# Kernel optimization log

Measured on AMD Instinct MI355X. Metric: run time of the kernel, lower is better.

The kernel has to match this reference:

```python
import jax, jax.numpy as jnp
import numpy as np

B, T, C, H = 2, 2048, 1024, 16
HD = C // H  # 64

def setup_inputs() -> dict:
    key = jax.random.key(0)
    ks = jax.random.split(key, 9)
    s = 0.02
    return {
        "x": jax.random.normal(ks[0], (B, T, C), jnp.float32),
        "Wq": jax.random.normal(ks[1], (C, C), jnp.float32) * s,
        "bq": jax.random.normal(ks[2], (C,), jnp.float32) * s,
        "Wk": jax.random.normal(ks[3], (C, C), jnp.float32) * s,
        "bk": jax.random.normal(ks[4], (C,), jnp.float32) * s,
        "Wv": jax.random.normal(ks[5], (C, C), jnp.float32) * s,
        "bv": jax.random.normal(ks[6], (C,), jnp.float32) * s,
        "Wp": jax.random.normal(ks[7], (C, C), jnp.float32) * s,
        "bp": jax.random.normal(ks[8], (C,), jnp.float32) * s,
    }

def reference(x, Wq, bq, Wk, bk, Wv, bv, Wp, bp):
    Bb, Tt, Cc = x.shape
    hd = Cc // H
    # project and split heads: [B, H, T, hd]
    def heads(W, b):
        return (x @ W.T + b).reshape(Bb, Tt, H, hd).transpose(0, 2, 1, 3)
    q, k, v = heads(Wq, bq), heads(Wk, bk), heads(Wv, bv)
    scale = 1.0 / np.sqrt(hd).astype(np.float32)
    att = jnp.einsum('bhqd,bhkd->bhqk', q, k) * scale
    causal = jnp.tril(jnp.ones((Tt, Tt), bool))
    att = jnp.where(causal[None, None], att, -jnp.inf)
    att = jax.nn.softmax(att, axis=-1)
    y = jnp.einsum('bhqk,bhkd->bhqd', att, v)
    y = y.transpose(0, 2, 1, 3).reshape(Bb, Tt, Cc)
    return y @ Wp.T + bp
```

## Files before the change

kernel.cpp:

```cpp
#include <hip/hip_runtime.h>
#include <hip/hip_bf16.h>

#define Tsz 2048
#define Csz 1024
#define Hn 16

typedef short s8v __attribute__((ext_vector_type(8)));
typedef short s4v __attribute__((ext_vector_type(4)));
typedef float f4v __attribute__((ext_vector_type(4)));
typedef int   i4v __attribute__((ext_vector_type(4)));
typedef unsigned u2v __attribute__((ext_vector_type(2)));

#define QSCALE (0.125f * 1.44269504088896f)

__device__ __forceinline__ unsigned short bfr(float x) {
    return (unsigned short)((__builtin_bit_cast(unsigned, x) + 0x8000u) >> 16);
}
__device__ __forceinline__ unsigned pack2_rn(float a, float b) {
    const unsigned ua = __builtin_bit_cast(unsigned, a) + 0x8000u;
    const unsigned ub = __builtin_bit_cast(unsigned, b) + 0x8000u;
    return (ua >> 16) | (ub & 0xFFFF0000u);
}

__device__ __forceinline__ void gload_lds(const void* g, void* l) {
    __builtin_amdgcn_global_load_lds(
        (const __attribute__((address_space(1))) void*)g,
        (__attribute__((address_space(3))) void*)l, 16, 0, 0);
}

__global__ void cvt6(const float* __restrict__ x, const float* __restrict__ wq,
                     const float* __restrict__ wk, const float* __restrict__ wv,
                     const float* __restrict__ wp,
                     short* __restrict__ xo, short* __restrict__ qo,
                     short* __restrict__ ko, short* __restrict__ vo,
                     short* __restrict__ po) {
    const int bx = blockIdx.x;
    const float* in; short* out; int ib;
    if (bx < 4096) { in = x; out = xo; ib = bx; }
    else {
        const int r = bx - 4096, w = r >> 10;
        ib = r & 1023;
        switch (w) {
            case 0: in = wq; out = qo; break;
            case 1: in = wk; out = ko; break;
            case 2: in = wv; out = vo; break;
            default: in = wp; out = po; break;
        }
    }
    const int i = ib * 1024 + threadIdx.x * 4;
    float4 v = *(const float4*)(in + i);
    int2 o;
    o.x = (int)pack2_rn(v.x, v.y);
    o.y = (int)pack2_rn(v.z, v.w);
    *(int2*)(out + i) = o;
}

__global__ __launch_bounds__(256, 3) void qkv_gemm(
    const short* __restrict__ X,
    const short* __restrict__ Wq, const short* __restrict__ Wk, const short* __restrict__ Wv,
    const float* __restrict__ bq, const float* __restrict__ bk, const float* __restrict__ bv,
    short* __restrict__ Qo, short* __restrict__ Ko, short* __restrict__ Vto)
{
    const int z = blockIdx.z;
    const short* W = (z == 0) ? Wq : (z == 1) ? Wk : Wv;
    const float* bias = (z == 0) ? bq : (z == 1) ? bk : bv;

    __shared__ __align__(16) short Ash[128 * 32];
    __shared__ __align__(16) short Bsh[128 * 32];
    __shared__ __align__(16) short TR[64 * 72];

    const int tid = threadIdx.x, lane = tid & 63, wave = tid >> 6;
    const int ln = lane & 15, hi = lane >> 4;
    const int m0 = blockIdx.x * 128, n0 = blockIdx.y * 128;
    const int wm = (wave >> 1) * 64, wn = (wave & 1) * 64;

    const short* Ag = X + (size_t)(m0 + (tid >> 2)) * Csz + (tid & 3) * 8;
    const short* Bg = W + (size_t)(n0 + (tid >> 2)) * Csz + (tid & 3) * 8;

    f4v acc[4][4];
    #pragma unroll
    for (int mt = 0; mt < 4; mt++)
        #pragma unroll
        for (int nt = 0; nt < 4; nt++)
            #pragma unroll
            for (int i = 0; i < 4; i++) acc[mt][nt][i] = 0.f;

    for (int k0 = 0; k0 < Csz; k0 += 32) {
        __syncthreads();
        gload_lds(Ag + k0, Ash + tid * 8);
        gload_lds(Ag + k0 + (size_t)64 * Csz, Ash + 2048 + tid * 8);
        gload_lds(Bg + k0, Bsh + tid * 8);
        gload_lds(Bg + k0 + (size_t)64 * Csz, Bsh + 2048 + tid * 8);
        __syncthreads();

        s8v af[4], bfr_[4];
        #pragma unroll
        for (int mt = 0; mt < 4; mt++)
            af[mt] = *(const s8v*)(Ash + (wm + mt * 16 + ln) * 32 + hi * 8);
        #pragma unroll
        for (int nt = 0; nt < 4; nt++)
            bfr_[nt] = *(const s8v*)(Bsh + (wn + nt * 16 + ln) * 32 + hi * 8);
        #pragma unroll
        for (int mt = 0; mt < 4; mt++)
            #pragma unroll
            for (int nt = 0; nt < 4; nt++)
                acc[mt][nt] = __builtin_amdgcn_mfma_f32_16x16x32_bf16(af[mt], bfr_[nt], acc[mt][nt], 0, 0, 0);
    }

    if (z == 2) {
        const int b = m0 >> 11, t0 = m0 & 2047;
        float bvv[4];
        #pragma unroll
        for (int nt = 0; nt < 4; nt++) bvv[nt] = bias[n0 + wn + nt * 16 + ln];
        #pragma unroll
        for (int ph = 0; ph < 4; ph++) {
            const int mh = ph >> 1, nh = ph & 1;
            __syncthreads();
            if ((wave >> 1) == mh && (wave & 1) == nh) {
                #pragma unroll
                for (int mt = 0; mt < 4; mt++)
                    #pragma unroll
                    for (int nt = 0; nt < 4; nt++) {
                        int2 pk;
                        pk.x = (int)pack2_rn(acc[mt][nt][0] + bvv[nt], acc[mt][nt][1] + bvv[nt]);
                        pk.y = (int)pack2_rn(acc[mt][nt][2] + bvv[nt], acc[mt][nt][3] + bvv[nt]);
                        *(int2*)(TR + (nt * 16 + ln) * 72 + mt * 16 + hi * 4) = pk;
                    }
            }
            __syncthreads();
            const int chl = tid >> 2, seg = tid & 3;
            const s8v r0 = *(const s8v*)(TR + chl * 72 + seg * 16);
            const s8v r1 = *(const s8v*)(TR + chl * 72 + seg * 16 + 8);
            short* dst = Vto + (size_t)(b * 1024 + n0 + nh * 64 + chl) * Tsz + t0 + mh * 64 + seg * 16;
            *(s8v*)(dst) = r0;
            *(s8v*)(dst + 8) = r1;
        }
        return;
    }

    const float scale = (z == 0) ? QSCALE : 1.0f;
    short* out = (z == 0) ? Qo : Ko;

    #pragma unroll
    for (int nt = 0; nt < 4; nt++) {
        const int col = n0 + wn + nt * 16 + ln;
        const float bvv = bias[col];
        #pragma unroll
        for (int mt = 0; mt < 4; mt++) {
            const int row0 = m0 + wm + mt * 16 + hi * 4;
            #pragma unroll
            for (int i = 0; i < 4; i++)
                out[(size_t)(row0 + i) * Csz + col] = (short)bfr((acc[mt][nt][i] + bvv) * scale);
        }
    }
}

__global__ __launch_bounds__(256, 2) void proj_gemm(
    const short* __restrict__ A, const short* __restrict__ W,
    const float* __restrict__ bias, float* __restrict__ out)
{
    __shared__ __align__(16) short Ash[128 * 32];
    __shared__ __align__(16) short Bsh[64 * 32];

    const int tid = threadIdx.x, lane = tid & 63, wave = tid >> 6;
    const int ln = lane & 15, hi = lane >> 4;
    const int m0 = blockIdx.x * 128, n0 = blockIdx.y * 64;
    const int wm = (wave >> 1) * 64, wn = (wave & 1) * 32;

    const short* Ag = A + (size_t)(m0 + (tid >> 2)) * Csz + (tid & 3) * 8;
    const short* Bg = W + (size_t)(n0 + (tid >> 2)) * Csz + (tid & 3) * 8;

    f4v acc[4][2];
    #pragma unroll
    for (int mt = 0; mt < 4; mt++)
        #pragma unroll
        for (int nt = 0; nt < 2; nt++)
            #pragma unroll
            for (int i = 0; i < 4; i++) acc[mt][nt][i] = 0.f;

    for (int k0 = 0; k0 < Csz; k0 += 32) {
        __syncthreads();
        gload_lds(Ag + k0, Ash + tid * 8);
        gload_lds(Ag + k0 + (size_t)64 * Csz, Ash + 2048 + tid * 8);
        gload_lds(Bg + k0, Bsh + tid * 8);
        __syncthreads();

        s8v af[4], bfr_[2];
        #pragma unroll
        for (int mt = 0; mt < 4; mt++)
            af[mt] = *(const s8v*)(Ash + (wm + mt * 16 + ln) * 32 + hi * 8);
        #pragma unroll
        for (int nt = 0; nt < 2; nt++)
            bfr_[nt] = *(const s8v*)(Bsh + (wn + nt * 16 + ln) * 32 + hi * 8);
        #pragma unroll
        for (int mt = 0; mt < 4; mt++)
            #pragma unroll
            for (int nt = 0; nt < 2; nt++)
                acc[mt][nt] = __builtin_amdgcn_mfma_f32_16x16x32_bf16(af[mt], bfr_[nt], acc[mt][nt], 0, 0, 0);
    }

    #pragma unroll
    for (int nt = 0; nt < 2; nt++) {
        const int col = n0 + wn + nt * 16 + ln;
        const float bvv = bias[col];
        #pragma unroll
        for (int mt = 0; mt < 4; mt++)
            #pragma unroll
            for (int i = 0; i < 4; i++)
                out[(size_t)(m0 + wm + mt * 16 + hi * 4 + i) * Csz + col] = acc[mt][nt][i] + bvv;
    }
}

__global__ __launch_bounds__(256, 3) void attn15(
    const short* __restrict__ Q, const short* __restrict__ Kg,
    const short* __restrict__ Vt, short* __restrict__ Y)
{
    __shared__ __align__(16) short SB[3][2][64 * 64];

    const int tid = threadIdx.x, lane = tid & 63, wave = tid >> 6;
    const int ln = lane & 15, hi = lane >> 4;

    const int n = blockIdx.x;
    const int c = n & 255, j = n >> 8;
    const int bh = (j << 3) | (c >> 5);
    const int t = c & 31;
    const int qt = (j & 1) ? t : 31 - t;

    const size_t base = (size_t)(bh >> 4) * Tsz * Csz + (size_t)(bh & 15) * 64;
    const size_t vtbase = (size_t)bh * 64 * Tsz;
    const int qrel = wave * 16 + ln;

    s8v qf[2];
    #pragma unroll
    for (int kk = 0; kk < 2; kk++)
        qf[kk] = *(const s8v*)(Q + base + (size_t)(qt * 64 + qrel) * Csz + kk * 32 + hi * 8);

    f4v o[4];
    float lsum = 0.f;
    #pragma unroll
    for (int dt = 0; dt < 4; dt++)
        #pragma unroll
        for (int i = 0; i < 4; i++) o[dt][i] = 0.f;

    const int sr = tid >> 3, scs = tid & 7;
    const int csw = (scs ^ (sr & 7)) * 8;
    const short* KpA = Kg + base + (size_t)sr * Csz + csw;
    const short* KpB = KpA + (size_t)32 * Csz;
    const short* VpA = Vt + vtbase + (size_t)sr * Tsz + csw;
    const short* VpB = VpA + (size_t)32 * Tsz;
    const int nkb = qt + 1;

    int foff[2][4];
    #pragma unroll
    for (int nt = 0; nt < 4; nt++)
        #pragma unroll
        for (int kk = 0; kk < 2; kk++)
            foff[kk][nt] = (nt * 16 + ln) * 64 + (((kk * 4 + hi) ^ (ln & 7)) * 8);

    #define STAGE(b, kb_) {                                              \
        const size_t ko_ = (size_t)(kb_) * 64;                           \
        gload_lds(KpA + ko_ * Csz, &SB[b][0][tid * 8]);                  \
        gload_lds(KpB + ko_ * Csz, &SB[b][0][2048 + tid * 8]);           \
        gload_lds(VpA + ko_,       &SB[b][1][tid * 8]);                  \
        gload_lds(VpB + ko_,       &SB[b][1][2048 + tid * 8]);           \
    }

    STAGE(0, 0);
    if (nkb > 1) {
        STAGE(1, 1);
        asm volatile("s_waitcnt vmcnt(4)" ::: "memory");
    } else {
        asm volatile("s_waitcnt vmcnt(0)" ::: "memory");
    }
    __builtin_amdgcn_s_barrier();

    int bcur = 0, bnext = 1, bnn = 2;
    for (int kb = 0; kb < nkb; kb++) {
        if (kb + 2 < nkb) STAGE(bnn, kb + 2);

        const short* Kl = SB[bcur][0];
        const short* Vl = SB[bcur][1];
        s8v kf[2][4], vf[2][4];
        #pragma unroll
        for (int nt = 0; nt < 4; nt++)
            #pragma unroll
            for (int kk = 0; kk < 2; kk++) {
                kf[kk][nt] = *(const s8v*)(&Kl[foff[kk][nt]]);
                vf[kk][nt] = *(const s8v*)(&Vl[foff[kk][nt]]);
            }

        f4v s[4];
        #pragma unroll
        for (int nt = 0; nt < 4; nt++) {
            #pragma unroll
            for (int i = 0; i < 4; i++) s[nt][i] = 0.f;
            s[nt] = __builtin_amdgcn_mfma_f32_16x16x32_bf16(kf[0][nt], qf[0], s[nt], 0, 0, 0);
            s[nt] = __builtin_amdgcn_mfma_f32_16x16x32_bf16(kf[1][nt], qf[1], s[nt], 0, 0, 0);
        }

        const bool dg = (kb == qt);
        unsigned pw[4][2];
        #pragma unroll
        for (int nt = 0; nt < 4; nt++) {
            float pv[4];
            #pragma unroll
            for (int i = 0; i < 4; i++) pv[i] = exp2f(s[nt][i]);
            if (dg) {
                const int kr = nt * 16 + hi * 4;
                #pragma unroll
                for (int i = 0; i < 4; i++)
                    if (kr + i > qrel) pv[i] = 0.f;
            }
            lsum += (pv[0] + pv[1]) + (pv[2] + pv[3]);
            pw[nt][0] = pack2_rn(pv[0], pv[1]);
            pw[nt][1] = pack2_rn(pv[2], pv[3]);
        }

        u2v r0a = __builtin_amdgcn_permlane32_swap(pw[0][0], pw[1][0], false, false);
        u2v r0b = __builtin_amdgcn_permlane16_swap(r0a[0], r0a[1], false, false);
        u2v r1a = __builtin_amdgcn_permlane32_swap(pw[0][1], pw[1][1], false, false);
        u2v r1b = __builtin_amdgcn_permlane16_swap(r1a[0], r1a[1], false, false);
        u2v r2a = __builtin_amdgcn_permlane32_swap(pw[2][0], pw[3][0], false, false);
        u2v r2b = __builtin_amdgcn_permlane16_swap(r2a[0], r2a[1], false, false);
        u2v r3a = __builtin_amdgcn_permlane32_swap(pw[2][1], pw[3][1], false, false);
        u2v r3b = __builtin_amdgcn_permlane16_swap(r3a[0], r3a[1], false, false);
        i4v p0 = { (int)r0b[0], (int)r1b[0], (int)r0b[1], (int)r1b[1] };
        i4v p1 = { (int)r2b[0], (int)r3b[0], (int)r2b[1], (int)r3b[1] };
        const s8v pb0 = __builtin_bit_cast(s8v, p0);
        const s8v pb1 = __builtin_bit_cast(s8v, p1);

        #pragma unroll
        for (int dt = 0; dt < 4; dt++) {
            o[dt] = __builtin_amdgcn_mfma_f32_16x16x32_bf16(vf[0][dt], pb0, o[dt], 0, 0, 0);
            o[dt] = __builtin_amdgcn_mfma_f32_16x16x32_bf16(vf[1][dt], pb1, o[dt], 0, 0, 0);
        }

        if (kb + 1 < nkb) {
            if (kb + 2 < nkb) asm volatile("s_waitcnt vmcnt(4)" ::: "memory");
            else              asm volatile("s_waitcnt vmcnt(0)" ::: "memory");
            __builtin_amdgcn_s_barrier();
        }
        const int tb = bcur; bcur = bnext; bnext = bnn; bnn = tb;
    }
    #undef STAGE

    float l = lsum;
    l += __shfl_xor(l, 16);
    l += __shfl_xor(l, 32);
    const float inv = 1.0f / l;
    const int qrow = qt * 64 + qrel;
    #pragma unroll
    for (int dt = 0; dt < 4; dt++) {
        int2 w;
        w.x = (int)pack2_rn(o[dt][0] * inv, o[dt][1] * inv);
        w.y = (int)pack2_rn(o[dt][2] * inv, o[dt][3] * inv);
        *(int2*)(Y + base + (size_t)qrow * Csz + dt * 16 + hi * 4) = w;
    }
}

extern "C" void kernel_launch(void* const* d_in, const int* in_sizes, int n_in,
                              void* d_out, int out_size, void* d_ws, size_t ws_size,
                              hipStream_t stream) {
    const float* x  = (const float*)d_in[0];
    const float* Wq = (const float*)d_in[1];
    const float* bq = (const float*)d_in[2];
    const float* Wk = (const float*)d_in[3];
    const float* bk = (const float*)d_in[4];
    const float* Wv = (const float*)d_in[5];
    const float* bv = (const float*)d_in[6];
    const float* Wp = (const float*)d_in[7];
    const float* bp = (const float*)d_in[8];

    char* ws = (char*)d_ws;
    short* Xb  = (short*)(ws);
    short* Wqb = (short*)(ws + (8u  << 20));
    short* Wkb = (short*)(ws + (10u << 20));
    short* Wvb = (short*)(ws + (12u << 20));
    short* Wpb = (short*)(ws + (14u << 20));
    short* Qb  = (short*)(ws + (16u << 20));
    short* Kb  = (short*)(ws + (24u << 20));
    short* Vtb = (short*)(ws + (32u << 20));
    short* Yb  = (short*)(ws + (40u << 20));

    hipLaunchKernelGGL(cvt6, dim3(8192), dim3(256), 0, stream,
                       x, Wq, Wk, Wv, Wp, Xb, Wqb, Wkb, Wvb, Wpb);

    hipLaunchKernelGGL(qkv_gemm, dim3(32, 8, 3), dim3(256), 0, stream,
                       Xb, Wqb, Wkb, Wvb, bq, bk, bv, Qb, Kb, Vtb);

    hipLaunchKernelGGL(attn15, dim3(1024), dim3(256), 0, stream, Qb, Kb, Vtb, Yb);

    hipLaunchKernelGGL(proj_gemm, dim3(32, 16), dim3(256), 0, stream, Yb, Wpb, bp, (float*)d_out);
}
```

Measured before the change: 186.5 us.

## Compute softmax row sums via MFMA and unroll attention loop by buffer rotation

The attention kernel now computes the softmax denominator with two extra MFMAs per tile against a ones vector, replacing the per-lane float adds and the closing cross-lane shuffles. The KV loop is unrolled three ways so the triple-buffer indices are compile-time constants, and the staging pointers are incremented in place instead of recomputed. The fp32-to-bf16 packing switches to the hardware conversion intrinsic. This trims VALU, shuffle and address arithmetic from the inner loop but adds matrix-core work and increases code size.

```diff
diff --git a/kernel.cpp b/kernel.cpp
--- a/kernel.cpp
+++ b/kernel.cpp
@@ -20,6 +20,12 @@
     const unsigned ua = __builtin_bit_cast(unsigned, a) + 0x8000u;
     const unsigned ub = __builtin_bit_cast(unsigned, b) + 0x8000u;
     return (ua >> 16) | (ub & 0xFFFF0000u);
+}
+__device__ __forceinline__ unsigned cvt2(float a, float b) {
+    __hip_bfloat162 h = __float22bfloat162_rn(float2{a, b});
+    unsigned r;
+    __builtin_memcpy(&r, &h, 4);
+    return r;
 }
 
 __device__ __forceinline__ void gload_lds(const void* g, void* l) {
@@ -211,7 +217,7 @@
     }
 }
 
-__global__ __launch_bounds__(256, 3) void attn15(
+__global__ __launch_bounds__(256, 3) void attn16(
     const short* __restrict__ Q, const short* __restrict__ Kg,
     const short* __restrict__ Vt, short* __restrict__ Y)
 {
@@ -236,18 +242,23 @@
         qf[kk] = *(const s8v*)(Q + base + (size_t)(qt * 64 + qrel) * Csz + kk * 32 + hi * 8);
 
     f4v o[4];
-    float lsum = 0.f;
+    f4v lacc;
+    #pragma unroll
+    for (int i = 0; i < 4; i++) lacc[i] = 0.f;
     #pragma unroll
     for (int dt = 0; dt < 4; dt++)
         #pragma unroll
         for (int i = 0; i < 4; i++) o[dt][i] = 0.f;
+
+    const s8v ones8 = { (short)0x3F80, (short)0x3F80, (short)0x3F80, (short)0x3F80,
+                        (short)0x3F80, (short)0x3F80, (short)0x3F80, (short)0x3F80 };
 
     const int sr = tid >> 3, scs = tid & 7;
     const int csw = (scs ^ (sr & 7)) * 8;
-    const short* KpA = Kg + base + (size_t)sr * Csz + csw;
-    const short* KpB = KpA + (size_t)32 * Csz;
-    const short* VpA = Vt + vtbase + (size_t)sr * Tsz + csw;
-    const short* VpB = VpA + (size_t)32 * Tsz;
+    const short* KsA = Kg + base + (size_t)sr * Csz + csw;
+    const short* KsB = KsA + (size_t)32 * Csz;
+    const short* VsA = Vt + vtbase + (size_t)sr * Tsz + csw;
+    const short* VsB = VsA + (size_t)32 * Tsz;
     const int nkb = qt + 1;
 
     int foff[2][4];
@@ -257,103 +268,95 @@
         for (int kk = 0; kk < 2; kk++)
             foff[kk][nt] = (nt * 16 + ln) * 64 + (((kk * 4 + hi) ^ (ln & 7)) * 8);
 
-    #define STAGE(b, kb_) {                                              \
-        const size_t ko_ = (size_t)(kb_) * 64;                           \
-        gload_lds(KpA + ko_ * Csz, &SB[b][0][tid * 8]);                  \
-        gload_lds(KpB + ko_ * Csz, &SB[b][0][2048 + tid * 8]);           \
-        gload_lds(VpA + ko_,       &SB[b][1][tid * 8]);                  \
-        gload_lds(VpB + ko_,       &SB[b][1][2048 + tid * 8]);           \
-    }
-
-    STAGE(0, 0);
+    #define STAGE3(B) {                                    \
+        gload_lds(KsA, &SB[B][0][tid * 8]);                \
+        gload_lds(KsB, &SB[B][0][2048 + tid * 8]);         \
+        gload_lds(VsA, &SB[B][1][tid * 8]);                \
+        gload_lds(VsB, &SB[B][1][2048 + tid * 8]);         \
+        KsA += (size_t)64 * Csz; KsB += (size_t)64 * Csz;  \
+        VsA += 64; VsB += 64;                              \
+    }
+
+    STAGE3(0);
     if (nkb > 1) {
-        STAGE(1, 1);
+        STAGE3(1);
         asm volatile("s_waitcnt vmcnt(4)" ::: "memory");
     } else {
         asm volatile("s_waitcnt vmcnt(0)" ::: "memory");
     }
     __builtin_amdgcn_s_barrier();
 
-    int bcur = 0, bnext = 1, bnn = 2;
-    for (int kb = 0; kb < nkb; kb++) {
-        if (kb + 2 < nkb) STAGE(bnn, kb + 2);
-
-        const short* Kl = SB[bcur][0];
-        const short* Vl = SB[bcur][1];
-        s8v kf[2][4], vf[2][4];
-        #pragma unroll
-        for (int nt = 0; nt < 4; nt++)
-            #pragma unroll
-            for (int kk = 0; kk < 2; kk++) {
-                kf[kk][nt] = *(const s8v*)(&Kl[foff[kk][nt]]);
-                vf[kk][nt] = *(const s8v*)(&Vl[foff[kk][nt]]);
-            }
-
-        f4v s[4];
-        #pragma unroll
-        for (int nt = 0; nt < 4; nt++) {
-            #pragma unroll
-            for (int i = 0; i < 4; i++) s[nt][i] = 0.f;
-            s[nt] = __builtin_amdgcn_mfma_f32_16x16x32_bf16(kf[0][nt], qf[0], s[nt], 0, 0, 0);
-            s[nt] = __builtin_amdgcn_mfma_f32_16x16x32_bf16(kf[1][nt], qf[1], s[nt], 0, 0, 0);
-        }
-
-        const bool dg = (kb == qt);
-        unsigned pw[4][2];
-        #pragma unroll
-        for (int nt = 0; nt < 4; nt++) {
-            float pv[4];
-            #pragma unroll
-            for (int i = 0; i < 4; i++) pv[i] = exp2f(s[nt][i]);
-            if (dg) {
-                const int kr = nt * 16 + hi * 4;
-                #pragma unroll
-                for (int i = 0; i < 4; i++)
-                    if (kr + i > qrel) pv[i] = 0.f;
-            }
-            lsum += (pv[0] + pv[1]) + (pv[2] + pv[3]);
-            pw[nt][0] = pack2_rn(pv[0], pv[1]);
-            pw[nt][1] = pack2_rn(pv[2], pv[3]);
-        }
-
-        u2v r0a = __builtin_amdgcn_permlane32_swap(pw[0][0], pw[1][0], false, false);
-        u2v r0b = __builtin_amdgcn_permlane16_swap(r0a[0], r0a[1], false, false);
-        u2v r1a = __builtin_amdgcn_permlane32_swap(pw[0][1], pw[1][1], false, false);
-        u2v r1b = __builtin_amdgcn_permlane16_swap(r1a[0], r1a[1], false, false);
-        u2v r2a = __builtin_amdgcn_permlane32_swap(pw[2][0], pw[3][0], false, false);
-        u2v r2b = __builtin_amdgcn_permlane16_swap(r2a[0], r2a[1], false, false);
-        u2v r3a = __builtin_amdgcn_permlane32_swap(pw[2][1], pw[3][1], false, false);
-        u2v r3b = __builtin_amdgcn_permlane16_swap(r3a[0], r3a[1], false, false);
-        i4v p0 = { (int)r0b[0], (int)r1b[0], (int)r0b[1], (int)r1b[1] };
-        i4v p1 = { (int)r2b[0], (int)r3b[0], (int)r2b[1], (int)r3b[1] };
-        const s8v pb0 = __builtin_bit_cast(s8v, p0);
-        const s8v pb1 = __builtin_bit_cast(s8v, p1);
-
-        #pragma unroll
-        for (int dt = 0; dt < 4; dt++) {
-            o[dt] = __builtin_amdgcn_mfma_f32_16x16x32_bf16(vf[0][dt], pb0, o[dt], 0, 0, 0);
-            o[dt] = __builtin_amdgcn_mfma_f32_16x16x32_bf16(vf[1][dt], pb1, o[dt], 0, 0, 0);
-        }
-
-        if (kb + 1 < nkb) {
-            if (kb + 2 < nkb) asm volatile("s_waitcnt vmcnt(4)" ::: "memory");
-            else              asm volatile("s_waitcnt vmcnt(0)" ::: "memory");
-            __builtin_amdgcn_s_barrier();
-        }
-        const int tb = bcur; bcur = bnext; bnext = bnn; bnn = tb;
-    }
-    #undef STAGE
-
-    float l = lsum;
-    l += __shfl_xor(l, 16);
-    l += __shfl_xor(l, 32);
-    const float inv = 1.0f / l;
+    #define TILE(B0, B2, kb_) {                                                     \
+        const bool st_ = (kb_) + 2 < nkb;                                           \
+        if (st_) STAGE3(B2);                                                        \
+        s8v kf[2][4], vf[2][4];                                                     \
+        for (int nt = 0; nt < 4; nt++) {                                            \
+            kf[0][nt] = *(const s8v*)(&SB[B0][0][foff[0][nt]]);                     \
+            kf[1][nt] = *(const s8v*)(&SB[B0][0][foff[1][nt]]);                     \
+            vf[0][nt] = *(const s8v*)(&SB[B0][1][foff[0][nt]]);                     \
+            vf[1][nt] = *(const s8v*)(&SB[B0][1][foff[1][nt]]);                     \
+        }                                                                           \
+        f4v s[4];                                                                   \
+        for (int nt = 0; nt < 4; nt++) {                                            \
+            for (int i = 0; i < 4; i++) s[nt][i] = 0.f;                             \
+            s[nt] = __builtin_amdgcn_mfma_f32_16x16x32_bf16(kf[0][nt], qf[0], s[nt], 0, 0, 0); \
+            s[nt] = __builtin_amdgcn_mfma_f32_16x16x32_bf16(kf[1][nt], qf[1], s[nt], 0, 0, 0); \
+        }                                                                           \
+        const bool dg_ = ((kb_) == qt);                                             \
+        unsigned pw[4][2];                                                          \
+        for (int nt = 0; nt < 4; nt++) {                                            \
+            float e0 = exp2f(s[nt][0]), e1 = exp2f(s[nt][1]);                       \
+            float e2 = exp2f(s[nt][2]), e3 = exp2f(s[nt][3]);                       \
+            if (dg_) {                                                              \
+                const int kr = nt * 16 + hi * 4;                                    \
+                if (kr + 0 > qrel) e0 = 0.f;                                        \
+                if (kr + 1 > qrel) e1 = 0.f;                                        \
+                if (kr + 2 > qrel) e2 = 0.f;                                        \
+                if (kr + 3 > qrel) e3 = 0.f;                                        \
+            }                                                                       \
+            pw[nt][0] = cvt2(e0, e1);                                               \
+            pw[nt][1] = cvt2(e2, e3);                                               \
+        }                                                                           \
+        u2v r0a = __builtin_amdgcn_permlane32_swap(pw[0][0], pw[1][0], false, false); \
+        u2v r0b = __builtin_amdgcn_permlane16_swap(r0a[0], r0a[1], false, false);   \
+        u2v r1a = __builtin_amdgcn_permlane32_swap(pw[0][1], pw[1][1], false, false); \
+        u2v r1b = __builtin_amdgcn_permlane16_swap(r1a[0], r1a[1], false, false);   \
+        u2v r2a = __builtin_amdgcn_permlane32_swap(pw[2][0], pw[3][0], false, false); \
+        u2v r2b = __builtin_amdgcn_permlane16_swap(r2a[0], r2a[1], false, false);   \
+        u2v r3a = __builtin_amdgcn_permlane32_swap(pw[2][1], pw[3][1], false, false); \
+        u2v r3b = __builtin_amdgcn_permlane16_swap(r3a[0], r3a[1], false, false);   \
+        i4v p0 = { (int)r0b[0], (int)r1b[0], (int)r0b[1], (int)r1b[1] };            \
+        i4v p1 = { (int)r2b[0], (int)r3b[0], (int)r2b[1], (int)r3b[1] };            \
+        const s8v pb0 = __builtin_bit_cast(s8v, p0);                                \
+        const s8v pb1 = __builtin_bit_cast(s8v, p1);                                \
+        for (int dt = 0; dt < 4; dt++) {                                            \
+            o[dt] = __builtin_amdgcn_mfma_f32_16x16x32_bf16(vf[0][dt], pb0, o[dt], 0, 0, 0); \
+            o[dt] = __builtin_amdgcn_mfma_f32_16x16x32_bf16(vf[1][dt], pb1, o[dt], 0, 0, 0); \
+        }                                                                           \
+        lacc = __builtin_amdgcn_mfma_f32_16x16x32_bf16(ones8, pb0, lacc, 0, 0, 0);  \
+        lacc = __builtin_amdgcn_mfma_f32_16x16x32_bf16(ones8, pb1, lacc, 0, 0, 0);  \
+        if ((kb_) + 1 < nkb) {                                                      \
+            if (st_) asm volatile("s_waitcnt vmcnt(4)" ::: "memory");               \
+            else     asm volatile("s_waitcnt vmcnt(0)" ::: "memory");               \
+            __builtin_amdgcn_s_barrier();                                           \
+        }                                                                           \
+    }
+
+    for (int kb = 0; kb < nkb; kb += 3) {
+        TILE(0, 2, kb);
+        if (kb + 1 < nkb) TILE(1, 0, kb + 1);
+        if (kb + 2 < nkb) TILE(2, 1, kb + 2);
+    }
+    #undef TILE
+    #undef STAGE3
+
+    const float inv = 1.0f / lacc[0];
     const int qrow = qt * 64 + qrel;
     #pragma unroll
     for (int dt = 0; dt < 4; dt++) {
         int2 w;
-        w.x = (int)pack2_rn(o[dt][0] * inv, o[dt][1] * inv);
-        w.y = (int)pack2_rn(o[dt][2] * inv, o[dt][3] * inv);
+        w.x = (int)cvt2(o[dt][0] * inv, o[dt][1] * inv);
+        w.y = (int)cvt2(o[dt][2] * inv, o[dt][3] * inv);
         *(int2*)(Y + base + (size_t)qrow * Csz + dt * 16 + hi * 4) = w;
     }
 }
@@ -388,7 +391,7 @@
     hipLaunchKernelGGL(qkv_gemm, dim3(32, 8, 3), dim3(256), 0, stream,
                        Xb, Wqb, Wkb, Wvb, bq, bk, bv, Qb, Kb, Vtb);
 
-    hipLaunchKernelGGL(attn15, dim3(1024), dim3(256), 0, stream, Qb, Kb, Vtb, Yb);
+    hipLaunchKernelGGL(attn16, dim3(1024), dim3(256), 0, stream, Qb, Kb, Vtb, Yb);
 
     hipLaunchKernelGGL(proj_gemm, dim3(32, 16), dim3(256), 0, stream, Yb, Wpb, bp, (float*)d_out);
 }
```

After: 187.3 us. No clear change (+0.4%).
